# Performance work log

Hardware: AMD Instinct MI355X
Metric: run time of the kernel (lower is better)

The kernel has to match this reference:

```python
import jax, jax.numpy as jnp
import numpy as np
from jax import lax

INPUT_DIM = 16
H1, H2 = 64, 32
OUT_DIM = 1
B, T = 4096, 168


def _uniform(key, shape, k):
    return jax.random.uniform(key, shape, jnp.float32, -k, k)


def setup_inputs() -> dict:
    key = jax.random.key(0)
    ks = jax.random.split(key, 12)
    k1 = 1.0 / np.sqrt(H1)
    k2 = 1.0 / np.sqrt(H2)
    return {
        "x": jax.random.normal(ks[0], (B, T, INPUT_DIM), jnp.float32),
        # layer 1 (PyTorch gate order: i, f, g, o)
        "W_ih1": _uniform(ks[1], (4 * H1, INPUT_DIM), k1),
        "W_hh1": _uniform(ks[2], (4 * H1, H1), k1),
        "b_ih1": _uniform(ks[3], (4 * H1,), k1),
        "b_hh1": _uniform(ks[4], (4 * H1,), k1),
        # layer 2
        "W_ih2": _uniform(ks[5], (4 * H2, H1), k2),
        "W_hh2": _uniform(ks[6], (4 * H2, H2), k2),
        "b_ih2": _uniform(ks[7], (4 * H2,), k2),
        "b_hh2": _uniform(ks[8], (4 * H2,), k2),
        # final linear
        "W_fc": _uniform(ks[9], (OUT_DIM, H2), k2),
        "b_fc": _uniform(ks[10], (OUT_DIM,), k2),
    }


def _lstm(x, W_ih, W_hh, b_ih, b_hh, hidden):
    # Precompute input-to-gate projections for all timesteps: [B, T, 4H]
    xg = jnp.einsum("btd,gd->btg", x, W_ih) + b_ih + b_hh

    def step(carry, xt):
        h, c = carry
        gates = xt + h @ W_hh.T  # [B, 4H]
        i, f, g, o = jnp.split(gates, 4, axis=-1)
        i = jax.nn.sigmoid(i)
        f = jax.nn.sigmoid(f)
        g = jnp.tanh(g)
        o = jax.nn.sigmoid(o)
        c = f * c + i * g
        h = o * jnp.tanh(c)
        return (h, c), h

    bsz = x.shape[0]
    init = (jnp.zeros((bsz, hidden), x.dtype), jnp.zeros((bsz, hidden), x.dtype))
    (_, _), hs = lax.scan(step, init, jnp.swapaxes(xg, 0, 1))  # hs: [T, B, H]
    return jnp.swapaxes(hs, 0, 1)  # [B, T, H]


def reference(x, W_ih1, W_hh1, b_ih1, b_hh1, W_ih2, W_hh2, b_ih2, b_hh2, W_fc, b_fc):
    # Dropout layers are identity at inference (p=0.2 in train only).
    h1 = _lstm(x, W_ih1, W_hh1, b_ih1, b_hh1, H1)   # [B, T, 64]
    h2 = _lstm(h1, W_ih2, W_hh2, b_ih2, b_hh2, H2)  # [B, T, 32]
    last = h2[:, -1, :]                              # [B, 32]
    return last @ W_fc.T + b_fc                      # [B, OUT_DIM]
```

## Files before the change

### kernel.cpp

```cpp
#include <hip/hip_runtime.h>


typedef __bf16 bf16x8 __attribute__((ext_vector_type(8)));
typedef float  f32x4  __attribute__((ext_vector_type(4)));

constexpr int T_SEQ = 168;
constexpr int DIN   = 16;
constexpr int NB    = 16;

__device__ __forceinline__ float fsig(float v)  { return __builtin_amdgcn_rcpf(1.f + __expf(-v)); }
__device__ __forceinline__ float ftanhf(float v){ return 2.f * __builtin_amdgcn_rcpf(1.f + __expf(-2.f * v)) - 1.f; }

__device__ __forceinline__ void split_bf16(float x, __bf16& hi, __bf16& lo) {
  hi = (__bf16)x;
  lo = (__bf16)(x - (float)hi);
}

__device__ __forceinline__ void load_frag8(const float* __restrict__ Wrow, int k0,
                                           bf16x8& hi, bf16x8& lo) {
#pragma unroll
  for (int j = 0; j < 8; ++j) {
    float v = Wrow[k0 + j];
    __bf16 h = (__bf16)v;
    hi[j] = h;
    lo[j] = (__bf16)(v - (float)h);
  }
}

#define MFMA(a, b, c) __builtin_amdgcn_mfma_f32_16x16x32_bf16((a), (b), (c), 0, 0, 0)

__global__ __launch_bounds__(512, 1)
void lstm_mfma_kernel(const float* __restrict__ x,
    const float* __restrict__ Wih1, const float* __restrict__ Whh1,
    const float* __restrict__ bih1, const float* __restrict__ bhh1,
    const float* __restrict__ Wih2, const float* __restrict__ Whh2,
    const float* __restrict__ bih2, const float* __restrict__ bhh2,
    const float* __restrict__ Wfc,  const float* __restrict__ bfc,
    float* __restrict__ out)
{
  __shared__ __align__(16) __bf16 sA1[2][4 * 64 * 8];
  __shared__ __align__(16) __bf16 sA2[2][2 * 64 * 8];
  __shared__ __align__(16) __bf16 sAX[2][2 * 64 * 8];
  __shared__ __align__(16) __bf16 sB2[8 * 4 * 64 * 8];
  __shared__ __align__(16) float  sH2f[16 * 32];

  const int tid  = threadIdx.x;
  const int w    = tid >> 6;
  const int lane = tid & 63;
  const int q    = lane >> 4;
  const int col  = lane & 15;
  const int b0   = blockIdx.x * NB;

  const bool isL1 = (w < 4);
  const bool isL2 = (w == 4) || (w == 5);
  const bool isXL = (w >= 6);
  const int  wl   = w - 4;

  bf16x8 bhh[4][4];
  bf16x8 bih[4];
  float  b1v[4] = {0.f, 0.f, 0.f, 0.f};
  if (isL1) {
#pragma unroll
    for (int g = 0; g < 4; ++g) {
      const int r = g * 64 + w * 16 + col;
      const float* Wr = Whh1 + r * 64;
      bf16x8 h0, l0, h1f, l1f;
      load_frag8(Wr, 0 * 32 + q * 8, h0, l0);
      load_frag8(Wr, 1 * 32 + q * 8, h1f, l1f);
      bhh[g][0] = h0; bhh[g][1] = h1f; bhh[g][2] = l0; bhh[g][3] = l1f;
      bf16x8 xh, xl;
      load_frag8(Wih1 + r * 16, (q & 1) * 8, xh, xl);
      bih[g] = (q < 2) ? xh : xl;
      b1v[g] = bih1[r] + bhh1[r];
    }
  }
  bf16x8 bh2[4][2];
  float  b2v[4] = {0.f, 0.f, 0.f, 0.f};
  if (isL2) {
#pragma unroll
    for (int g = 0; g < 4; ++g) {
      const int r = g * 32 + wl * 16 + col;
      bf16x8 hh, ll;
      load_frag8(Whh2 + r * 32, q * 8, hh, ll);
      bh2[g][0] = hh; bh2[g][1] = ll;
      b2v[g] = bih2[r] + bhh2[r];
    }
  }

  for (int idx = tid; idx < 8 * 4 * 64; idx += 512) {
    const int nt = idx >> 8;
    const int kb = (idx >> 6) & 3;
    const int ln = idx & 63;
    const int qq = ln >> 4, cc = ln & 15;
    const int g  = nt >> 1, wv = nt & 1;
    const int r  = g * 32 + wv * 16 + cc;
    const int k0 = (kb & 1) * 32 + qq * 8;
    bf16x8 hh, ll;
    load_frag8(Wih2 + r * 64, k0, hh, ll);
    *(bf16x8*)&sB2[((nt * 4 + kb) * 64 + ln) * 8] = (kb < 2) ? hh : ll;
  }

  {
    bf16x8 z;
#pragma unroll
    for (int j = 0; j < 8; ++j) z[j] = (__bf16)0.f;
    for (int i = tid; i < 2 * 4 * 64; i += 512) *(bf16x8*)&sA1[0][i * 8] = z;
    for (int i = tid; i < 2 * 2 * 64; i += 512) *(bf16x8*)&sA2[0][i * 8] = z;
    for (int i = tid; i < 2 * 2 * 64; i += 512) *(bf16x8*)&sAX[0][i * 8] = z;
  }
  const int xi = tid - 384;
  const int bx = (xi >> 3) & 15;
  const int d2 = (xi & 7) * 2;
  if (isXL) {
    const float2 xv = *(const float2*)&x[((size_t)(b0 + bx) * T_SEQ + 0) * DIN + d2];
    const float vv[2] = {xv.x, xv.y};
#pragma unroll
    for (int s = 0; s < 2; ++s) {
      const int d = d2 + s;
      __bf16 xh, xl; split_bf16(vv[s], xh, xl);
      sAX[0][(0 * 64 + (d >> 3) * 16 + bx) * 8 + (d & 7)]       = xh;
      sAX[0][(0 * 64 + (2 + (d >> 3)) * 16 + bx) * 8 + (d & 7)] = xl;
      sAX[0][(1 * 64 + (d >> 3) * 16 + bx) * 8 + (d & 7)]       = xl;
      sAX[0][(1 * 64 + (2 + (d >> 3)) * 16 + bx) * 8 + (d & 7)] = xh;
    }
  }
  __syncthreads();

  float c1s[4] = {0.f, 0.f, 0.f, 0.f};
  float c2s[4] = {0.f, 0.f, 0.f, 0.f};
  const int uu  = w * 16 + col;
  const int uu2 = wl * 16 + col;

  for (int t = 0; t <= T_SEQ; ++t) {
    const int p = t & 1;

    if (isL1 && t < T_SEQ) {
      bf16x8 a1[4], ax0, ax1;
#pragma unroll
      for (int kb = 0; kb < 4; ++kb) a1[kb] = *(const bf16x8*)&sA1[p][(kb * 64 + lane) * 8];
      ax0 = *(const bf16x8*)&sAX[p][(0 * 64 + lane) * 8];
      ax1 = *(const bf16x8*)&sAX[p][(1 * 64 + lane) * 8];

      f32x4 c[4];
#pragma unroll
      for (int g = 0; g < 4; ++g) { c[g][0] = b1v[g]; c[g][1] = b1v[g]; c[g][2] = b1v[g]; c[g][3] = b1v[g]; }
#pragma unroll
      for (int g = 0; g < 4; ++g) {
        c[g] = MFMA(ax0, bih[g], c[g]);
        c[g] = MFMA(ax1, bih[g], c[g]);
#pragma unroll
        for (int kb = 0; kb < 4; ++kb) {
          c[g] = MFMA(a1[kb],     bhh[g][kb], c[g]);
          c[g] = MFMA(a1[kb ^ 2], bhh[g][kb], c[g]);
        }
      }
      const int kbh = uu >> 5;
      const int lnb = ((uu & 31) >> 3) * 16;
      const int jj  = uu & 7;
#pragma unroll
      for (int r = 0; r < 4; ++r) {
        const float iv = fsig(c[0][r]);
        const float fv = fsig(c[1][r]);
        const float gv = ftanhf(c[2][r]);
        const float ov = fsig(c[3][r]);
        const float cc = fmaf(fv, c1s[r], iv * gv);
        c1s[r] = cc;
        __bf16 hh, hl;
        split_bf16(ov * ftanhf(cc), hh, hl);
        const int m = q * 4 + r;
        sA1[1 - p][((kbh * 64) + lnb + m) * 8 + jj]       = hh;
        sA1[1 - p][(((2 + kbh) * 64) + lnb + m) * 8 + jj] = hl;
      }
    }

    if (isL2 && t >= 1) {
      bf16x8 a2[4], ah0, ah1;
#pragma unroll
      for (int kb = 0; kb < 4; ++kb) a2[kb] = *(const bf16x8*)&sA1[p][(kb * 64 + lane) * 8];
      ah0 = *(const bf16x8*)&sA2[p][(0 * 64 + lane) * 8];
      ah1 = *(const bf16x8*)&sA2[p][(1 * 64 + lane) * 8];

      f32x4 c2[4];
#pragma unroll
      for (int g = 0; g < 4; ++g) { c2[g][0] = b2v[g]; c2[g][1] = b2v[g]; c2[g][2] = b2v[g]; c2[g][3] = b2v[g]; }
#pragma unroll
      for (int g = 0; g < 4; ++g) {
        const int nt = g * 2 + wl;
#pragma unroll
        for (int kb = 0; kb < 4; ++kb) {
          const bf16x8 bb = *(const bf16x8*)&sB2[((nt * 4 + kb) * 64 + lane) * 8];
          c2[g] = MFMA(a2[kb],     bb, c2[g]);
          c2[g] = MFMA(a2[kb ^ 2], bb, c2[g]);
        }
        c2[g] = MFMA(ah0, bh2[g][0], c2[g]);
        c2[g] = MFMA(ah1, bh2[g][1], c2[g]);
        c2[g] = MFMA(ah1, bh2[g][0], c2[g]);
        c2[g] = MFMA(ah0, bh2[g][1], c2[g]);
      }
      const int lnb2 = ((uu2 & 31) >> 3) * 16;
      const int jj2  = uu2 & 7;
#pragma unroll
      for (int r = 0; r < 4; ++r) {
        const float iv = fsig(c2[0][r]);
        const float fv = fsig(c2[1][r]);
        const float gv = ftanhf(c2[2][r]);
        const float ov = fsig(c2[3][r]);
        const float cc = fmaf(fv, c2s[r], iv * gv);
        c2s[r] = cc;
        const float hf = ov * ftanhf(cc);
        __bf16 hh, hl;
        split_bf16(hf, hh, hl);
        const int m = q * 4 + r;
        sA2[1 - p][((0 * 64) + lnb2 + m) * 8 + jj2] = hh;
        sA2[1 - p][((1 * 64) + lnb2 + m) * 8 + jj2] = hl;
        if (t == T_SEQ) sH2f[m * 32 + uu2] = hf;
      }
    }

    if (isXL && t + 1 < T_SEQ) {
      const float2 xv = *(const float2*)&x[((size_t)(b0 + bx) * T_SEQ + (t + 1)) * DIN + d2];
      const float vv[2] = {xv.x, xv.y};
#pragma unroll
      for (int s = 0; s < 2; ++s) {
        const int d = d2 + s;
        __bf16 xh, xl; split_bf16(vv[s], xh, xl);
        sAX[1 - p][(0 * 64 + (d >> 3) * 16 + bx) * 8 + (d & 7)]       = xh;
        sAX[1 - p][(0 * 64 + (2 + (d >> 3)) * 16 + bx) * 8 + (d & 7)] = xl;
        sAX[1 - p][(1 * 64 + (d >> 3) * 16 + bx) * 8 + (d & 7)]       = xl;
        sAX[1 - p][(1 * 64 + (2 + (d >> 3)) * 16 + bx) * 8 + (d & 7)] = xh;
      }
    }

    __syncthreads();
  }

  if (tid < NB) {
    float s = bfc[0];
#pragma unroll
    for (int j = 0; j < 32; ++j) s = fmaf(Wfc[j], sH2f[tid * 32 + j], s);
    out[b0 + tid] = s;
  }
}

extern "C" void kernel_launch(void* const* d_in, const int* in_sizes, int n_in,
                              void* d_out, int out_size, void* d_ws, size_t ws_size,
                              hipStream_t stream) {
  (void)in_sizes; (void)n_in; (void)out_size; (void)d_ws; (void)ws_size;
  const float* x    = (const float*)d_in[0];
  const float* Wih1 = (const float*)d_in[1];
  const float* Whh1 = (const float*)d_in[2];
  const float* bih1 = (const float*)d_in[3];
  const float* bhh1 = (const float*)d_in[4];
  const float* Wih2 = (const float*)d_in[5];
  const float* Whh2 = (const float*)d_in[6];
  const float* bih2 = (const float*)d_in[7];
  const float* bhh2 = (const float*)d_in[8];
  const float* Wfc  = (const float*)d_in[9];
  const float* bfc  = (const float*)d_in[10];
  float* out = (float*)d_out;

  hipLaunchKernelGGL(lstm_mfma_kernel, dim3(4096 / NB), dim3(512), 0, stream,
                     x, Wih1, Whh1, bih1, bhh1, Wih2, Whh2, bih2, bhh2, Wfc, bfc, out);
}
```

Before: 300.2 us.

## Split layer-2 MFMA work across two wave groups and load x directly into registers

Repurposes the two x-loader waves as a second layer-2 group that computes partial gate products (the low-part input terms and the recurrent terms) and passes them through shared memory. The other layer-2 waves compute the high-part input terms and then apply the activations. Layer-2 input weights now live in registers instead of a shared-memory table. Layer-1 waves prefetch x from global memory themselves and split it into bf16 hi/lo parts, and layer 1 drops the lo×lo correction MFMAs. Each timestep now needs a second block-wide barrier, and dropping the lo×lo terms slightly changes numerics.

```diff
diff --git a/kernel.cpp b/kernel.cpp
--- a/kernel.cpp
+++ b/kernel.cpp
@@ -5,7 +5,6 @@
 typedef float  f32x4  __attribute__((ext_vector_type(4)));
 
 constexpr int T_SEQ = 168;
-constexpr int DIN   = 16;
 constexpr int NB    = 16;
 
 __device__ __forceinline__ float fsig(float v)  { return __builtin_amdgcn_rcpf(1.f + __expf(-v)); }
@@ -40,8 +39,7 @@
 {
   __shared__ __align__(16) __bf16 sA1[2][4 * 64 * 8];
   __shared__ __align__(16) __bf16 sA2[2][2 * 64 * 8];
-  __shared__ __align__(16) __bf16 sAX[2][2 * 64 * 8];
-  __shared__ __align__(16) __bf16 sB2[8 * 4 * 64 * 8];
+  __shared__ __align__(16) float  sP[2 * 4 * 64 * 4];
   __shared__ __align__(16) float  sH2f[16 * 32];
 
   const int tid  = threadIdx.x;
@@ -51,10 +49,11 @@
   const int col  = lane & 15;
   const int b0   = blockIdx.x * NB;
 
-  const bool isL1 = (w < 4);
-  const bool isL2 = (w == 4) || (w == 5);
-  const bool isXL = (w >= 6);
-  const int  wl   = w - 4;
+  const bool isL1  = (w < 4);
+  const bool isL2b = (w == 4) || (w == 5);
+  const bool isL2a = (w >= 6);
+  const int  wl2b  = w - 4;
+  const int  wl2a  = w - 6;
 
   bf16x8 bhh[4][4];
   bf16x8 bih[4];
@@ -74,30 +73,37 @@
       b1v[g] = bih1[r] + bhh1[r];
     }
   }
-  bf16x8 bh2[4][2];
+  bf16x8 w2h_[4][2], w2l_[4][2];
   float  b2v[4] = {0.f, 0.f, 0.f, 0.f};
-  if (isL2) {
+  if (isL2b) {
 #pragma unroll
     for (int g = 0; g < 4; ++g) {
-      const int r = g * 32 + wl * 16 + col;
+      const int r = g * 32 + wl2b * 16 + col;
+#pragma unroll
+      for (int kb = 0; kb < 2; ++kb) {
+        bf16x8 hh, ll;
+        load_frag8(Wih2 + r * 64, kb * 32 + q * 8, hh, ll);
+        w2h_[g][kb] = hh; w2l_[g][kb] = ll;
+      }
+      b2v[g] = bih2[r] + bhh2[r];
+    }
+  }
+  bf16x8 w2a[4][2];
+  bf16x8 bh2h[4], bh2l[4];
+  if (isL2a) {
+#pragma unroll
+    for (int g = 0; g < 4; ++g) {
+      const int r = g * 32 + wl2a * 16 + col;
+#pragma unroll
+      for (int kb = 0; kb < 2; ++kb) {
+        bf16x8 hh, ll;
+        load_frag8(Wih2 + r * 64, kb * 32 + q * 8, hh, ll);
+        w2a[g][kb] = hh;
+      }
       bf16x8 hh, ll;
       load_frag8(Whh2 + r * 32, q * 8, hh, ll);
-      bh2[g][0] = hh; bh2[g][1] = ll;
-      b2v[g] = bih2[r] + bhh2[r];
-    }
-  }
-
-  for (int idx = tid; idx < 8 * 4 * 64; idx += 512) {
-    const int nt = idx >> 8;
-    const int kb = (idx >> 6) & 3;
-    const int ln = idx & 63;
-    const int qq = ln >> 4, cc = ln & 15;
-    const int g  = nt >> 1, wv = nt & 1;
-    const int r  = g * 32 + wv * 16 + cc;
-    const int k0 = (kb & 1) * 32 + qq * 8;
-    bf16x8 hh, ll;
-    load_frag8(Wih2 + r * 64, k0, hh, ll);
-    *(bf16x8*)&sB2[((nt * 4 + kb) * 64 + ln) * 8] = (kb < 2) ? hh : ll;
+      bh2h[g] = hh; bh2l[g] = ll;
+    }
   }
 
   {
@@ -106,53 +112,90 @@
     for (int j = 0; j < 8; ++j) z[j] = (__bf16)0.f;
     for (int i = tid; i < 2 * 4 * 64; i += 512) *(bf16x8*)&sA1[0][i * 8] = z;
     for (int i = tid; i < 2 * 2 * 64; i += 512) *(bf16x8*)&sA2[0][i * 8] = z;
-    for (int i = tid; i < 2 * 2 * 64; i += 512) *(bf16x8*)&sAX[0][i * 8] = z;
-  }
-  const int xi = tid - 384;
-  const int bx = (xi >> 3) & 15;
-  const int d2 = (xi & 7) * 2;
-  if (isXL) {
-    const float2 xv = *(const float2*)&x[((size_t)(b0 + bx) * T_SEQ + 0) * DIN + d2];
-    const float vv[2] = {xv.x, xv.y};
-#pragma unroll
-    for (int s = 0; s < 2; ++s) {
-      const int d = d2 + s;
-      __bf16 xh, xl; split_bf16(vv[s], xh, xl);
-      sAX[0][(0 * 64 + (d >> 3) * 16 + bx) * 8 + (d & 7)]       = xh;
-      sAX[0][(0 * 64 + (2 + (d >> 3)) * 16 + bx) * 8 + (d & 7)] = xl;
-      sAX[0][(1 * 64 + (d >> 3) * 16 + bx) * 8 + (d & 7)]       = xl;
-      sAX[0][(1 * 64 + (2 + (d >> 3)) * 16 + bx) * 8 + (d & 7)] = xh;
-    }
   }
   __syncthreads();
+
+  const float* xbase = x + ((size_t)(b0 + col) * T_SEQ) * 16 + (q & 1) * 8;
+  float4 xcA, xcB, xnA, xnB;
+  if (isL1) {
+    xcA = *(const float4*)(xbase + 0);
+    xcB = *(const float4*)(xbase + 4);
+  }
 
   float c1s[4] = {0.f, 0.f, 0.f, 0.f};
   float c2s[4] = {0.f, 0.f, 0.f, 0.f};
-  const int uu  = w * 16 + col;
-  const int uu2 = wl * 16 + col;
+  const int uu   = w * 16 + col;
+  const int uu2b = wl2b * 16 + col;
 
   for (int t = 0; t <= T_SEQ; ++t) {
     const int p = t & 1;
 
+    if (isL1 && t + 1 < T_SEQ) {
+      const float* xr = xbase + (size_t)(t + 1) * 16;
+      xnA = *(const float4*)(xr + 0);
+      xnB = *(const float4*)(xr + 4);
+    }
+
+    if (isL2a && t >= 1) {
+      const bf16x8 a2l0 = *(const bf16x8*)&sA1[p][(2 * 64 + lane) * 8];
+      const bf16x8 a2l1 = *(const bf16x8*)&sA1[p][(3 * 64 + lane) * 8];
+      const bf16x8 ah0  = *(const bf16x8*)&sA2[p][(0 * 64 + lane) * 8];
+      const bf16x8 ah1  = *(const bf16x8*)&sA2[p][(1 * 64 + lane) * 8];
+#pragma unroll
+      for (int g = 0; g < 4; ++g) {
+        f32x4 pa = {0.f, 0.f, 0.f, 0.f};
+        pa = MFMA(a2l0, w2a[g][0], pa);
+        pa = MFMA(a2l1, w2a[g][1], pa);
+        pa = MFMA(ah0,  bh2h[g],  pa);
+        pa = MFMA(ah1,  bh2h[g],  pa);
+        pa = MFMA(ah0,  bh2l[g],  pa);
+        *(f32x4*)&sP[((wl2a * 4 + g) * 64 + lane) * 4] = pa;
+      }
+    }
+
+    f32x4 c2[4];
+    if (isL2b && t >= 1) {
+      const bf16x8 a2h0 = *(const bf16x8*)&sA1[p][(0 * 64 + lane) * 8];
+      const bf16x8 a2h1 = *(const bf16x8*)&sA1[p][(1 * 64 + lane) * 8];
+#pragma unroll
+      for (int g = 0; g < 4; ++g) {
+        c2[g][0] = b2v[g]; c2[g][1] = b2v[g]; c2[g][2] = b2v[g]; c2[g][3] = b2v[g];
+        c2[g] = MFMA(a2h0, w2h_[g][0], c2[g]);
+        c2[g] = MFMA(a2h1, w2h_[g][1], c2[g]);
+        c2[g] = MFMA(a2h0, w2l_[g][0], c2[g]);
+        c2[g] = MFMA(a2h1, w2l_[g][1], c2[g]);
+      }
+    }
+    __syncthreads();
+
     if (isL1 && t < T_SEQ) {
-      bf16x8 a1[4], ax0, ax1;
+      const float xc[8] = {xcA.x, xcA.y, xcA.z, xcA.w, xcB.x, xcB.y, xcB.z, xcB.w};
+      bf16x8 xh8, xl8;
+#pragma unroll
+      for (int j = 0; j < 8; ++j) {
+        __bf16 h, l; split_bf16(xc[j], h, l);
+        xh8[j] = h; xl8[j] = l;
+      }
+      const bf16x8 ax0 = (q < 2) ? xh8 : xl8;
+      const bf16x8 ax1 = (q < 2) ? xl8 : xh8;
+
+      bf16x8 a1[4];
 #pragma unroll
       for (int kb = 0; kb < 4; ++kb) a1[kb] = *(const bf16x8*)&sA1[p][(kb * 64 + lane) * 8];
-      ax0 = *(const bf16x8*)&sAX[p][(0 * 64 + lane) * 8];
-      ax1 = *(const bf16x8*)&sAX[p][(1 * 64 + lane) * 8];
 
       f32x4 c[4];
 #pragma unroll
       for (int g = 0; g < 4; ++g) { c[g][0] = b1v[g]; c[g][1] = b1v[g]; c[g][2] = b1v[g]; c[g][3] = b1v[g]; }
 #pragma unroll
       for (int g = 0; g < 4; ++g) {
-        c[g] = MFMA(ax0, bih[g], c[g]);
-        c[g] = MFMA(ax1, bih[g], c[g]);
-#pragma unroll
-        for (int kb = 0; kb < 4; ++kb) {
-          c[g] = MFMA(a1[kb],     bhh[g][kb], c[g]);
-          c[g] = MFMA(a1[kb ^ 2], bhh[g][kb], c[g]);
-        }
+        c[g] = MFMA(ax0,   bih[g],    c[g]);
+        c[g] = MFMA(ax1,   bih[g],    c[g]);
+        c[g] = MFMA(a1[0], bhh[g][0], c[g]);
+        c[g] = MFMA(a1[1], bhh[g][1], c[g]);
+        c[g] = MFMA(a1[2], bhh[g][0], c[g]);
+        c[g] = MFMA(a1[3], bhh[g][1], c[g]);
+        c[g] = MFMA(a1[0], bhh[g][2], c[g]);
+        c[g] = MFMA(a1[1], bhh[g][3], c[g]);
       }
       const int kbh = uu >> 5;
       const int lnb = ((uu & 31) >> 3) * 16;
@@ -171,34 +214,15 @@
         sA1[1 - p][((kbh * 64) + lnb + m) * 8 + jj]       = hh;
         sA1[1 - p][(((2 + kbh) * 64) + lnb + m) * 8 + jj] = hl;
       }
-    }
-
-    if (isL2 && t >= 1) {
-      bf16x8 a2[4], ah0, ah1;
-#pragma unroll
-      for (int kb = 0; kb < 4; ++kb) a2[kb] = *(const bf16x8*)&sA1[p][(kb * 64 + lane) * 8];
-      ah0 = *(const bf16x8*)&sA2[p][(0 * 64 + lane) * 8];
-      ah1 = *(const bf16x8*)&sA2[p][(1 * 64 + lane) * 8];
-
-      f32x4 c2[4];
-#pragma unroll
-      for (int g = 0; g < 4; ++g) { c2[g][0] = b2v[g]; c2[g][1] = b2v[g]; c2[g][2] = b2v[g]; c2[g][3] = b2v[g]; }
-#pragma unroll
-      for (int g = 0; g < 4; ++g) {
-        const int nt = g * 2 + wl;
-#pragma unroll
-        for (int kb = 0; kb < 4; ++kb) {
-          const bf16x8 bb = *(const bf16x8*)&sB2[((nt * 4 + kb) * 64 + lane) * 8];
-          c2[g] = MFMA(a2[kb],     bb, c2[g]);
-          c2[g] = MFMA(a2[kb ^ 2], bb, c2[g]);
-        }
-        c2[g] = MFMA(ah0, bh2[g][0], c2[g]);
-        c2[g] = MFMA(ah1, bh2[g][1], c2[g]);
-        c2[g] = MFMA(ah1, bh2[g][0], c2[g]);
-        c2[g] = MFMA(ah0, bh2[g][1], c2[g]);
-      }
-      const int lnb2 = ((uu2 & 31) >> 3) * 16;
-      const int jj2  = uu2 & 7;
+      xcA = xnA; xcB = xnB;
+    }
+
+    if (isL2b && t >= 1) {
+      const int lnb2 = ((uu2b & 31) >> 3) * 16;
+      const int jj2  = uu2b & 7;
+#pragma unroll
+      for (int g = 0; g < 4; ++g)
+        c2[g] += *(const f32x4*)&sP[((wl2b * 4 + g) * 64 + lane) * 4];
 #pragma unroll
       for (int r = 0; r < 4; ++r) {
         const float iv = fsig(c2[0][r]);
@@ -213,24 +237,9 @@
         const int m = q * 4 + r;
         sA2[1 - p][((0 * 64) + lnb2 + m) * 8 + jj2] = hh;
         sA2[1 - p][((1 * 64) + lnb2 + m) * 8 + jj2] = hl;
-        if (t == T_SEQ) sH2f[m * 32 + uu2] = hf;
-      }
-    }
-
-    if (isXL && t + 1 < T_SEQ) {
-      const float2 xv = *(const float2*)&x[((size_t)(b0 + bx) * T_SEQ + (t + 1)) * DIN + d2];
-      const float vv[2] = {xv.x, xv.y};
-#pragma unroll
-      for (int s = 0; s < 2; ++s) {
-        const int d = d2 + s;
-        __bf16 xh, xl; split_bf16(vv[s], xh, xl);
-        sAX[1 - p][(0 * 64 + (d >> 3) * 16 + bx) * 8 + (d & 7)]       = xh;
-        sAX[1 - p][(0 * 64 + (2 + (d >> 3)) * 16 + bx) * 8 + (d & 7)] = xl;
-        sAX[1 - p][(1 * 64 + (d >> 3) * 16 + bx) * 8 + (d & 7)]       = xl;
-        sAX[1 - p][(1 * 64 + (2 + (d >> 3)) * 16 + bx) * 8 + (d & 7)] = xh;
-      }
-    }
-
+        if (t == T_SEQ) sH2f[m * 32 + uu2b] = hf;
+      }
+    }
     __syncthreads();
   }
 
```

Result: slower. 590.6 us (+96.8%).
